# Kernel tuning notes

Measured on AMD Instinct MI355X. Metric: run time of the kernel, lower is better.

The kernel has to match this reference:

```python
import jax, jax.numpy as jnp
import numpy as np

N = 100000      # nodes
E = 1600000     # edges (avg degree 16)
IN = 128        # in_features
HID = 128       # hidden
C = 40          # num_classes
G = 64          # graphs in batch


def _glorot(key, fan_in, fan_out):
    s = np.sqrt(6.0 / (fan_in + fan_out)).astype(np.float32)
    return jax.random.uniform(key, (fan_in, fan_out), minval=-s, maxval=s, dtype=jnp.float32)


def setup_inputs() -> dict:
    key = jax.random.key(0)
    ks = jax.random.split(key, 10)
    x = jax.random.normal(ks[0], (N, IN), dtype=jnp.float32)
    edge_index = jax.random.randint(ks[1], (2, E), 0, N, dtype=jnp.int32)
    edge_weight = jax.random.uniform(ks[2], (E,), dtype=jnp.float32)
    batch = jnp.sort(jax.random.randint(ks[3], (N,), 0, G, dtype=jnp.int32))
    W1 = _glorot(ks[4], IN, HID); b1 = jnp.zeros((HID,), jnp.float32)
    W2 = _glorot(ks[5], HID, HID); b2 = jnp.zeros((HID,), jnp.float32)
    W3 = _glorot(ks[6], HID, C);  b3 = jnp.zeros((C,), jnp.float32)
    return {"x": x, "edge_index": edge_index, "edge_weight": edge_weight,
            "batch": batch, "W1": W1, "b1": b1, "W2": W2, "b2": b2,
            "W3": W3, "b3": b3}


def _gin_layer(h, src, dst, w, W, b):
    # message: w_ij * h_j, scatter-add to destination, GIN eps=0, MLP = single Linear
    msg = h[src] * w[:, None]                                   # [E, D]
    agg = jax.ops.segment_sum(msg, dst, num_segments=h.shape[0])  # [N, D]
    return (h + agg) @ W + b


def reference(x, edge_index, edge_weight, batch, W1, b1, W2, b2, W3, b3):
    src, dst = edge_index[0], edge_index[1]
    h = jax.nn.relu(_gin_layer(x, src, dst, edge_weight, W1, b1))  # dropout p=0 -> identity
    h = jax.nn.relu(_gin_layer(h, src, dst, edge_weight, W2, b2))
    h = _gin_layer(h, src, dst, edge_weight, W3, b3)
    # global_add_pool over graph ids
    return jax.ops.segment_sum(h, batch, num_segments=G)          # [G, C]
```

## Files before the change

### kernel.cpp

```cpp
#include <hip/hip_runtime.h>


typedef __attribute__((ext_vector_type(8))) short short8;
typedef __attribute__((ext_vector_type(4))) float f32x4;

__device__ __forceinline__ unsigned short f2bf(float f) {
    unsigned u = __builtin_bit_cast(unsigned, f);
    u += 0x7fff + ((u >> 16) & 1);
    return (unsigned short)(u >> 16);
}
__device__ __forceinline__ float bf2f(unsigned short s) {
    unsigned u = (unsigned)s << 16;
    return __builtin_bit_cast(float, u);
}
__device__ __forceinline__ float bflo(unsigned u) {
    return __builtin_bit_cast(float, u << 16);
}
__device__ __forceinline__ float bfhi(unsigned u) {
    return __builtin_bit_cast(float, u & 0xffff0000u);
}
__device__ __forceinline__ unsigned packbf(float a, float b) {
    return (unsigned)f2bf(a) | ((unsigned)f2bf(b) << 16);
}

#define BKT_SHIFT 8
#define BKT_NODES 256
#define PCHUNK 4096
#define SB_CAP 7168

__global__ __launch_bounds__(256) void bucket_hist(const int* __restrict__ dst,
                                                   int* __restrict__ bh, int E_) {
    __shared__ int lh[512];
    for (int i = threadIdx.x; i < 512; i += 256) lh[i] = 0;
    __syncthreads();
    for (int i = blockIdx.x * 256 + threadIdx.x; i < E_; i += gridDim.x * 256)
        atomicAdd(&lh[dst[i] >> BKT_SHIFT], 1);
    __syncthreads();
    for (int i = threadIdx.x; i < 512; i += 256)
        if (lh[i]) atomicAdd(&bh[i], lh[i]);
}

__global__ __launch_bounds__(512) void bucket_scan(const int* __restrict__ bh,
                                                   int* __restrict__ bstart,
                                                   int* __restrict__ gcur,
                                                   int* __restrict__ rp,
                                                   int NB, int N_, int E_) {
    __shared__ int sd[512];
    const int tid = threadIdx.x;
    int v = (tid < NB) ? bh[tid] : 0;
    sd[tid] = v;
    __syncthreads();
    for (int ofs = 1; ofs < 512; ofs <<= 1) {
        int t = (tid >= ofs) ? sd[tid - ofs] : 0;
        __syncthreads();
        sd[tid] += t;
        __syncthreads();
    }
    int excl = sd[tid] - v;
    if (tid < NB) { bstart[tid] = excl; gcur[tid] = excl; }
    if (tid == NB - 1) bstart[NB] = excl + v;
    if (tid == 0) rp[N_] = E_;
}

__global__ __launch_bounds__(256) void partition_edges(const int* __restrict__ src,
                                                       const int* __restrict__ dst,
                                                       const float* __restrict__ ew,
                                                       int* __restrict__ gcur,
                                                       uint2* __restrict__ temp, int E_) {
    __shared__ int lcur[512];
    __shared__ int lexcl[512];
    __shared__ int gbase[512];
    __shared__ unsigned short bof[PCHUNK];
    __shared__ uint2 stag[PCHUNK];
    __shared__ int sd[256];
    const int tid = threadIdx.x;
    const int e0  = blockIdx.x * PCHUNK;
    const int n   = min(PCHUNK, E_ - e0);

    for (int i = tid; i < 512; i += 256) lcur[i] = 0;
    __syncthreads();
    for (int i = tid; i < n; i += 256)
        atomicAdd(&lcur[dst[e0 + i] >> BKT_SHIFT], 1);
    __syncthreads();
    const int a0 = lcur[2 * tid], a1 = lcur[2 * tid + 1];
    const int ps = a0 + a1;
    sd[tid] = ps;
    __syncthreads();
    for (int ofs = 1; ofs < 256; ofs <<= 1) {
        int t = (tid >= ofs) ? sd[tid - ofs] : 0;
        __syncthreads();
        sd[tid] += t;
        __syncthreads();
    }
    const int pexcl = sd[tid] - ps;
    __syncthreads();
    lexcl[2 * tid] = pexcl;      lexcl[2 * tid + 1] = pexcl + a0;
    lcur [2 * tid] = pexcl;      lcur [2 * tid + 1] = pexcl + a0;
    __syncthreads();
    for (int i = tid; i < n; i += 256) {
        int   s = src[e0 + i], d = dst[e0 + i];
        float wv = ew[e0 + i];
        int b = d >> BKT_SHIFT;
        int p = atomicAdd(&lcur[b], 1);
        stag[p].x = (unsigned)s | ((unsigned)(d & (BKT_NODES - 1)) << 17);
        stag[p].y = __float_as_uint(wv);
        bof[p] = (unsigned short)b;
    }
    __syncthreads();
    if (a0) gbase[2 * tid]     = atomicAdd(&gcur[2 * tid],     a0);
    if (a1) gbase[2 * tid + 1] = atomicAdd(&gcur[2 * tid + 1], a1);
    __syncthreads();
    for (int i = tid; i < n; i += 256) {
        int b = bof[i];
        temp[gbase[b] + (i - lexcl[b])] = stag[i];
    }
}

__global__ __launch_bounds__(256) void sort_bucket(const uint2* __restrict__ temp,
                                                   const int* __restrict__ bstart,
                                                   uint2* __restrict__ csr,
                                                   int* __restrict__ rp, int N_) {
    __shared__ int h[256], hcur[256], sd[256];
    __shared__ uint2 outb[SB_CAP];
    const int b = blockIdx.x, tid = threadIdx.x;
    const int lo = bstart[b], hi = bstart[b + 1];
    const int L = hi - lo;
    h[tid] = 0;
    __syncthreads();
    for (int i = tid; i < L; i += 256)
        atomicAdd(&h[(temp[lo + i].x >> 17) & (BKT_NODES - 1)], 1);
    __syncthreads();
    int v = h[tid];
    sd[tid] = v;
    __syncthreads();
    for (int ofs = 1; ofs < 256; ofs <<= 1) {
        int t = (tid >= ofs) ? sd[tid - ofs] : 0;
        __syncthreads();
        sd[tid] += t;
        __syncthreads();
    }
    const int excl = sd[tid] - v;
    hcur[tid] = excl;
    const int node = b * BKT_NODES + tid;
    if (node <= N_) rp[node] = lo + excl;
    __syncthreads();
    for (int i = tid; i < L; i += 256) {
        uint2 p = temp[lo + i];
        int pos = atomicAdd(&hcur[(p.x >> 17) & (BKT_NODES - 1)], 1);
        outb[pos] = p;
    }
    __syncthreads();
    for (int i = tid; i < L; i += 256) csr[lo + i] = outb[i];
}

__global__ __launch_bounds__(256) void convert_bf16(const float* __restrict__ in,
                                                    unsigned short* __restrict__ out, int n8) {
    int i = blockIdx.x * 256 + threadIdx.x;
    if (i >= n8) return;
    const float4* in4 = (const float4*)in;
    float4 a = in4[(size_t)i * 2], b = in4[(size_t)i * 2 + 1];
    short8 o;
    o[0] = (short)f2bf(a.x); o[1] = (short)f2bf(a.y);
    o[2] = (short)f2bf(a.z); o[3] = (short)f2bf(a.w);
    o[4] = (short)f2bf(b.x); o[5] = (short)f2bf(b.y);
    o[6] = (short)f2bf(b.z); o[7] = (short)f2bf(b.w);
    ((short8*)out)[i] = o;
}

__global__ __launch_bounds__(256) void pack_w(const float* __restrict__ W,
                                              unsigned short* __restrict__ Wp) {
    int idx = blockIdx.x * 256 + threadIdx.x;
    int j = idx & 7, lane = (idx >> 3) & 63, kg = (idx >> 9) & 3, cf = idx >> 11;
    int k = kg * 32 + ((lane >> 4) & 3) * 8 + j;
    int c = cf * 16 + (lane & 15);
    Wp[idx] = f2bf(W[k * 128 + c]);
}

__global__ __launch_bounds__(256) void aggregate_bf16(const unsigned short* __restrict__ H,
                                                      const int* __restrict__ rp,
                                                      const int2* __restrict__ csr,
                                                      unsigned short* __restrict__ Out, int n) {
    const int node = blockIdx.x * 4 + (threadIdx.x >> 6);
    const int lane = threadIdx.x & 63;
    if (node >= n) return;
    const int qid   = lane >> 4;
    const int qlane = lane & 15;
    const uint4* H4 = (const uint4*)H;

    uint4 self = H4[(size_t)node * 16 + qlane];

    float acc[8];
#pragma unroll
    for (int i = 0; i < 8; i++) acc[i] = 0.f;

    const int e0 = rp[node], e1 = rp[node + 1];
    for (int base = e0; base < e1; base += 64) {
        const int cnt = min(64, e1 - base);
        int   sv = 0;
        float wv = 0.f;
        if (base + lane < e1) {
            int2 p = csr[base + lane];
            sv = p.x & 0x1FFFF;
            wv = __int_as_float(p.y);
        }
        const int g4 = (cnt + 3) >> 2;
#pragma unroll 4
        for (int jg = 0; jg < g4; jg++) {
            int   j  = jg * 4 + qid;
            int   sj = __shfl(sv, j);
            float wj = __shfl(wv, j);
            uint4 v  = H4[(size_t)sj * 16 + qlane];
            acc[0] += wj * bflo(v.x); acc[1] += wj * bfhi(v.x);
            acc[2] += wj * bflo(v.y); acc[3] += wj * bfhi(v.y);
            acc[4] += wj * bflo(v.z); acc[5] += wj * bfhi(v.z);
            acc[6] += wj * bflo(v.w); acc[7] += wj * bfhi(v.w);
        }
    }

#pragma unroll
    for (int i = 0; i < 8; i++) {
        acc[i] += __shfl_xor(acc[i], 16);
        acc[i] += __shfl_xor(acc[i], 32);
    }

    if (qid == 0) {
        acc[0] += bflo(self.x); acc[1] += bfhi(self.x);
        acc[2] += bflo(self.y); acc[3] += bfhi(self.y);
        acc[4] += bflo(self.z); acc[5] += bfhi(self.z);
        acc[6] += bflo(self.w); acc[7] += bfhi(self.w);
        uint4 o;
        o.x = packbf(acc[0], acc[1]);
        o.y = packbf(acc[2], acc[3]);
        o.z = packbf(acc[4], acc[5]);
        o.w = packbf(acc[6], acc[7]);
        ((uint4*)Out)[(size_t)node * 16 + qlane] = o;
    }
}

__global__ __launch_bounds__(256) void gemm_mfma_bias_relu(const unsigned short* __restrict__ A,
                                                           const unsigned short* __restrict__ Wp,
                                                           const float* __restrict__ bias,
                                                           unsigned short* __restrict__ Out,
                                                           int nrows) {
    const int wave = threadIdx.x >> 6;
    const int lane = threadIdx.x & 63;
    const int rbase = blockIdx.x * 64 + wave * 16;
    const int arow = rbase + (lane & 15);
    const int arow_c = min(arow, nrows - 1);

    const short8* Arow = (const short8*)(A + (size_t)arow_c * 128);
    short8 a[4];
#pragma unroll
    for (int kg = 0; kg < 4; kg++) a[kg] = Arow[kg * 4 + (lane >> 4)];

    const short8* Bp = (const short8*)Wp;
    const int drow = rbase + ((lane >> 4) << 2);
    const int dcol = lane & 15;
#pragma unroll
    for (int cf = 0; cf < 8; cf++) {
        f32x4 acc = {0.f, 0.f, 0.f, 0.f};
#pragma unroll
        for (int kg = 0; kg < 4; kg++) {
            short8 b = Bp[(cf * 4 + kg) * 64 + lane];
            acc = __builtin_amdgcn_mfma_f32_16x16x32_bf16(a[kg], b, acc, 0, 0, 0);
        }
        float bv = bias[cf * 16 + dcol];
#pragma unroll
        for (int i = 0; i < 4; i++) {
            int r = drow + i;
            if (r < nrows) {
                float v = fmaxf(acc[i] + bv, 0.f);
                Out[(size_t)r * 128 + cf * 16 + dcol] = f2bf(v);
            }
        }
    }
}

__global__ __launch_bounds__(256) void graph_count(const int* __restrict__ batch,
                                                   int* __restrict__ cnt, int n) {
    int t  = blockIdx.x * 256 + threadIdx.x;
    int i0 = t * 16;
    if (i0 >= n) return;
    int end = min(i0 + 16, n);
    int g = batch[i0], c = 0;
    for (int i = i0; i < end; i++) {
        int gi = batch[i];
        if (gi != g) { atomicAdd(&cnt[g], c); g = gi; c = 0; }
        c++;
    }
    atomicAdd(&cnt[g], c);
}

__global__ __launch_bounds__(256) void pool_nodes(const unsigned short* __restrict__ H,
                                                  const int* __restrict__ batch,
                                                  float* __restrict__ P, int n) {
    const int k2 = threadIdx.x & 63;
    const int wv = threadIdx.x >> 6;
    int r = blockIdx.x * 64 + wv;
    const int end = min(blockIdx.x * 64 + 64, n);
    if (r >= end) return;
    const unsigned* H32 = (const unsigned*)H;
    float ax = 0.f, ay = 0.f;
    int gcur = batch[r];
    for (; r < end; r += 4) {
        int g = batch[r];
        if (g != gcur) {
            atomicAdd(&P[gcur * 128 + 2 * k2], ax);
            atomicAdd(&P[gcur * 128 + 2 * k2 + 1], ay);
            ax = ay = 0.f;
            gcur = g;
        }
        unsigned v = H32[(size_t)r * 64 + k2];
        ax += bflo(v);
        ay += bfhi(v);
    }
    atomicAdd(&P[gcur * 128 + 2 * k2], ax);
    atomicAdd(&P[gcur * 128 + 2 * k2 + 1], ay);
}

__global__ __launch_bounds__(256) void final_kernel(const float* __restrict__ P,
                                                    const float* __restrict__ W3,
                                                    const float* __restrict__ b3,
                                                    const int* __restrict__ cnt,
                                                    float* __restrict__ out, int total) {
    int idx = blockIdx.x * 256 + threadIdx.x;
    if (idx >= total) return;
    int g = idx / 40, c = idx % 40;
    float acc = (float)cnt[g] * b3[c];
    for (int kk = 0; kk < 128; kk++) acc += P[g * 128 + kk] * W3[kk * 40 + c];
    out[idx] = acc;
}

extern "C" void kernel_launch(void* const* d_in, const int* in_sizes, int n_in,
                              void* d_out, int out_size, void* d_ws, size_t ws_size,
                              hipStream_t stream) {
    const float* x     = (const float*)d_in[0];
    const int*   ei    = (const int*)d_in[1];
    const float* ew    = (const float*)d_in[2];
    const int*   batch = (const int*)d_in[3];
    const float* W1    = (const float*)d_in[4];
    const float* b1    = (const float*)d_in[5];
    const float* W2    = (const float*)d_in[6];
    const float* b2    = (const float*)d_in[7];
    const float* W3    = (const float*)d_in[8];
    const float* b3    = (const float*)d_in[9];
    float*       out   = (float*)d_out;

    const int E_ = in_sizes[2];
    const int N_ = in_sizes[3];
    const int* srcp = ei;
    const int* dstp = ei + E_;
    const int NB = (N_ + BKT_NODES - 1) >> BKT_SHIFT;

    char*  w   = (char*)d_ws;
    size_t off = 0;
    auto take = [&](size_t bytes) -> char* {
        char* p = w + off;
        off = (off + bytes + 255) & ~(size_t)255;
        return p;
    };
    unsigned short* xb  = (unsigned short*)take((size_t)N_ * 128 * 2);
    unsigned short* Ha  = (unsigned short*)take((size_t)N_ * 128 * 2);
    unsigned short* Hb  = (unsigned short*)take((size_t)N_ * 128 * 2);
    int*   rp      = (int*)take((size_t)(N_ + 1) * 4);
    uint2* tempE   = (uint2*)take((size_t)E_ * 8);
    uint2* csr     = (uint2*)take((size_t)E_ * 8);
    int*   bh      = (int*)take(512 * 4);
    int*   bstart  = (int*)take(513 * 4);
    int*   gcur    = (int*)take(512 * 4);
    float* P       = (float*)take(64 * 128 * 4);
    int*   cnt     = (int*)take(64 * 4);
    unsigned short* W1p = (unsigned short*)take(16384 * 2);
    unsigned short* W2p = (unsigned short*)take(16384 * 2);
    (void)ws_size; (void)n_in;

    hipMemsetAsync(bh, 0, 512 * 4, stream);
    bucket_hist<<<1024, 256, 0, stream>>>(dstp, bh, E_);
    bucket_scan<<<1, 512, 0, stream>>>(bh, bstart, gcur, rp, NB, N_, E_);
    partition_edges<<<(E_ + PCHUNK - 1) / PCHUNK, 256, 0, stream>>>(srcp, dstp, ew,
                                                                    gcur, tempE, E_);
    sort_bucket<<<NB, 256, 0, stream>>>(tempE, bstart, csr, rp, N_);

    convert_bf16<<<(N_ * 16 + 255) / 256, 256, 0, stream>>>(x, xb, N_ * 16);
    pack_w<<<64, 256, 0, stream>>>(W1, W1p);
    pack_w<<<64, 256, 0, stream>>>(W2, W2p);

    const int agrid = (N_ + 3) / 4;
    const int ggrid = (N_ + 63) / 64;
    aggregate_bf16<<<agrid, 256, 0, stream>>>(xb, rp, (const int2*)csr, Ha, N_);
    gemm_mfma_bias_relu<<<ggrid, 256, 0, stream>>>(Ha, W1p, b1, Hb, N_);
    aggregate_bf16<<<agrid, 256, 0, stream>>>(Hb, rp, (const int2*)csr, Ha, N_);
    gemm_mfma_bias_relu<<<ggrid, 256, 0, stream>>>(Ha, W2p, b2, Hb, N_);
    aggregate_bf16<<<agrid, 256, 0, stream>>>(Hb, rp, (const int2*)csr, Ha, N_);

    hipMemsetAsync(P, 0, 64 * 128 * 4 + 64 * 4, stream);
    graph_count<<<((N_ + 15) / 16 + 255) / 256, 256, 0, stream>>>(batch, cnt, N_);
    pool_nodes<<<(N_ + 63) / 64, 256, 0, stream>>>(Ha, batch, P, N_);
    final_kernel<<<(out_size + 255) / 256, 256, 0, stream>>>(P, W3, b3, cnt, out, out_size);
}
```

Before: 364.7 us.

## Fuse neighbor aggregation with MFMA linear layer via shared-memory tile

Combines the per-node gather-aggregate and the bf16 MFMA GEMM+bias+ReLU into one 1024-thread kernel. Each block aggregates 16 nodes into LDS, then 8 waves each compute one 16-column slice of the output. This removes the write and re-read of the aggregated intermediate and two kernel launches. It also switches the CSR edge reads to nontemporal loads. In exchange, half the waves sit idle during the GEMM phase, and the large blocks with a barrier may lower occupancy and latency hiding for the irregular gathers.

```diff
diff --git a/kernel.cpp b/kernel.cpp
--- a/kernel.cpp
+++ b/kernel.cpp
@@ -176,32 +176,21 @@
     Wp[idx] = f2bf(W[k * 128 + c]);
 }
 
-__global__ __launch_bounds__(256) void aggregate_bf16(const unsigned short* __restrict__ H,
-                                                      const int* __restrict__ rp,
-                                                      const int2* __restrict__ csr,
-                                                      unsigned short* __restrict__ Out, int n) {
-    const int node = blockIdx.x * 4 + (threadIdx.x >> 6);
-    const int lane = threadIdx.x & 63;
-    if (node >= n) return;
-    const int qid   = lane >> 4;
-    const int qlane = lane & 15;
-    const uint4* H4 = (const uint4*)H;
-
-    uint4 self = H4[(size_t)node * 16 + qlane];
-
-    float acc[8];
-#pragma unroll
-    for (int i = 0; i < 8; i++) acc[i] = 0.f;
-
+__device__ __forceinline__ void agg_node(const uint4* __restrict__ H4,
+                                         const int* __restrict__ rp,
+                                         const uint2* __restrict__ csr,
+                                         int node, int lane, int qid, int qlane,
+                                         float acc[8]) {
     const int e0 = rp[node], e1 = rp[node + 1];
     for (int base = e0; base < e1; base += 64) {
         const int cnt = min(64, e1 - base);
         int   sv = 0;
         float wv = 0.f;
         if (base + lane < e1) {
-            int2 p = csr[base + lane];
-            sv = p.x & 0x1FFFF;
-            wv = __int_as_float(p.y);
+            unsigned long long pv = __builtin_nontemporal_load(
+                (const unsigned long long*)csr + (base + lane));
+            sv = (int)((unsigned)pv & 0x1FFFF);
+            wv = __builtin_bit_cast(float, (unsigned)(pv >> 32));
         }
         const int g4 = (cnt + 3) >> 2;
 #pragma unroll 4
@@ -216,12 +205,93 @@
             acc[6] += wj * bflo(v.w); acc[7] += wj * bfhi(v.w);
         }
     }
-
 #pragma unroll
     for (int i = 0; i < 8; i++) {
         acc[i] += __shfl_xor(acc[i], 16);
         acc[i] += __shfl_xor(acc[i], 32);
     }
+}
+
+__global__ __launch_bounds__(1024) void agg_gemm(const unsigned short* __restrict__ H,
+                                                 const int* __restrict__ rp,
+                                                 const uint2* __restrict__ csr,
+                                                 const unsigned short* __restrict__ Wp,
+                                                 const float* __restrict__ bias,
+                                                 unsigned short* __restrict__ Out,
+                                                 int n) {
+    __shared__ unsigned Ag[16][68];
+    const int wv   = threadIdx.x >> 6;
+    const int lane = threadIdx.x & 63;
+    const int qid = lane >> 4, qlane = lane & 15;
+    const int node = blockIdx.x * 16 + wv;
+    const uint4* H4 = (const uint4*)H;
+
+    if (node < n) {
+        uint4 self = H4[(size_t)node * 16 + qlane];
+        float acc[8];
+#pragma unroll
+        for (int i = 0; i < 8; i++) acc[i] = 0.f;
+        agg_node(H4, rp, csr, node, lane, qid, qlane, acc);
+        if (qid == 0) {
+            acc[0] += bflo(self.x); acc[1] += bfhi(self.x);
+            acc[2] += bflo(self.y); acc[3] += bfhi(self.y);
+            acc[4] += bflo(self.z); acc[5] += bfhi(self.z);
+            acc[6] += bflo(self.w); acc[7] += bfhi(self.w);
+            uint4 o;
+            o.x = packbf(acc[0], acc[1]);
+            o.y = packbf(acc[2], acc[3]);
+            o.z = packbf(acc[4], acc[5]);
+            o.w = packbf(acc[6], acc[7]);
+            *(uint4*)&Ag[wv][qlane * 4] = o;
+        }
+    } else if (qid == 0) {
+        uint4 z = {0u, 0u, 0u, 0u};
+        *(uint4*)&Ag[wv][qlane * 4] = z;
+    }
+    __syncthreads();
+
+    if (wv < 8) {
+        const int row = lane & 15, hi = lane >> 4;
+        short8 a[4];
+#pragma unroll
+        for (int kg = 0; kg < 4; kg++) {
+            uint4 t = *(const uint4*)&Ag[row][kg * 16 + hi * 4];
+            a[kg] = __builtin_bit_cast(short8, t);
+        }
+        const short8* Bp = (const short8*)Wp;
+        f32x4 accv = {0.f, 0.f, 0.f, 0.f};
+#pragma unroll
+        for (int kg = 0; kg < 4; kg++) {
+            short8 b = Bp[(wv * 4 + kg) * 64 + lane];
+            accv = __builtin_amdgcn_mfma_f32_16x16x32_bf16(a[kg], b, accv, 0, 0, 0);
+        }
+        const float bvv = bias[wv * 16 + row];
+        const int drow = blockIdx.x * 16 + hi * 4;
+        const int dcol = wv * 16 + row;
+#pragma unroll
+        for (int i = 0; i < 4; i++) {
+            int r = drow + i;
+            if (r < n)
+                Out[(size_t)r * 128 + dcol] = f2bf(fmaxf(accv[i] + bvv, 0.f));
+        }
+    }
+}
+
+__global__ __launch_bounds__(256) void aggregate_bf16(const unsigned short* __restrict__ H,
+                                                      const int* __restrict__ rp,
+                                                      const uint2* __restrict__ csr,
+                                                      unsigned short* __restrict__ Out, int n) {
+    const int node = blockIdx.x * 4 + (threadIdx.x >> 6);
+    const int lane = threadIdx.x & 63;
+    if (node >= n) return;
+    const int qid = lane >> 4, qlane = lane & 15;
+    const uint4* H4 = (const uint4*)H;
+
+    uint4 self = H4[(size_t)node * 16 + qlane];
+    float acc[8];
+#pragma unroll
+    for (int i = 0; i < 8; i++) acc[i] = 0.f;
+    agg_node(H4, rp, csr, node, lane, qid, qlane, acc);
 
     if (qid == 0) {
         acc[0] += bflo(self.x); acc[1] += bfhi(self.x);
@@ -234,45 +304,6 @@
         o.z = packbf(acc[4], acc[5]);
         o.w = packbf(acc[6], acc[7]);
         ((uint4*)Out)[(size_t)node * 16 + qlane] = o;
-    }
-}
-
-__global__ __launch_bounds__(256) void gemm_mfma_bias_relu(const unsigned short* __restrict__ A,
-                                                           const unsigned short* __restrict__ Wp,
-                                                           const float* __restrict__ bias,
-                                                           unsigned short* __restrict__ Out,
-                                                           int nrows) {
-    const int wave = threadIdx.x >> 6;
-    const int lane = threadIdx.x & 63;
-    const int rbase = blockIdx.x * 64 + wave * 16;
-    const int arow = rbase + (lane & 15);
-    const int arow_c = min(arow, nrows - 1);
-
-    const short8* Arow = (const short8*)(A + (size_t)arow_c * 128);
-    short8 a[4];
-#pragma unroll
-    for (int kg = 0; kg < 4; kg++) a[kg] = Arow[kg * 4 + (lane >> 4)];
-
-    const short8* Bp = (const short8*)Wp;
-    const int drow = rbase + ((lane >> 4) << 2);
-    const int dcol = lane & 15;
-#pragma unroll
-    for (int cf = 0; cf < 8; cf++) {
-        f32x4 acc = {0.f, 0.f, 0.f, 0.f};
-#pragma unroll
-        for (int kg = 0; kg < 4; kg++) {
-            short8 b = Bp[(cf * 4 + kg) * 64 + lane];
-            acc = __builtin_amdgcn_mfma_f32_16x16x32_bf16(a[kg], b, acc, 0, 0, 0);
-        }
-        float bv = bias[cf * 16 + dcol];
-#pragma unroll
-        for (int i = 0; i < 4; i++) {
-            int r = drow + i;
-            if (r < nrows) {
-                float v = fmaxf(acc[i] + bv, 0.f);
-                Out[(size_t)r * 128 + cf * 16 + dcol] = f2bf(v);
-            }
-        }
     }
 }
 
@@ -385,16 +416,14 @@
     pack_w<<<64, 256, 0, stream>>>(W1, W1p);
     pack_w<<<64, 256, 0, stream>>>(W2, W2p);
 
+    const int fgrid = (N_ + 15) / 16;
     const int agrid = (N_ + 3) / 4;
-    const int ggrid = (N_ + 63) / 64;
-    aggregate_bf16<<<agrid, 256, 0, stream>>>(xb, rp, (const int2*)csr, Ha, N_);
-    gemm_mfma_bias_relu<<<ggrid, 256, 0, stream>>>(Ha, W1p, b1, Hb, N_);
-    aggregate_bf16<<<agrid, 256, 0, stream>>>(Hb, rp, (const int2*)csr, Ha, N_);
-    gemm_mfma_bias_relu<<<ggrid, 256, 0, stream>>>(Ha, W2p, b2, Hb, N_);
-    aggregate_bf16<<<agrid, 256, 0, stream>>>(Hb, rp, (const int2*)csr, Ha, N_);
+    agg_gemm<<<fgrid, 1024, 0, stream>>>(xb, rp, csr, W1p, b1, Hb, N_);
+    agg_gemm<<<fgrid, 1024, 0, stream>>>(Hb, rp, csr, W2p, b2, Ha, N_);
+    aggregate_bf16<<<agrid, 256, 0, stream>>>(Ha, rp, csr, Hb, N_);
 
     hipMemsetAsync(P, 0, 64 * 128 * 4 + 64 * 4, stream);
     graph_count<<<((N_ + 15) / 16 + 255) / 256, 256, 0, stream>>>(batch, cnt, N_);
-    pool_nodes<<<(N_ + 63) / 64, 256, 0, stream>>>(Ha, batch, P, N_);
+    pool_nodes<<<(N_ + 63) / 64, 256, 0, stream>>>(Hb, batch, P, N_);
     final_kernel<<<(out_size + 255) / 256, 256, 0, stream>>>(P, W3, b3, cnt, out, out_size);
 }
```

After: 372.0 us. +2.0%, slower.
